# Performance work log

Measured on AMD Instinct MI355X. Metric: run time of the kernel, lower is better.

## Reference

```python
import jax, jax.numpy as jnp
import numpy as np

EPS = 1e-5
GROUPS = 16


def _deform_conv_gn(input, offset, mask, weight, bias, gamma, beta):
    # Modulated deformable conv v2 (k=3, stride=1, pad=1) + GroupNorm(16).
    B, C, H, W = input.shape
    Co = weight.shape[0]
    K = 9
    # kernel taps relative to center (pad=1 cancels the -1 origin shift)
    ky = jnp.repeat(jnp.arange(3) - 1, 3).astype(input.dtype)   # [9]
    kx = jnp.tile(jnp.arange(3) - 1, 3).astype(input.dtype)     # [9]
    off = offset.reshape(B, K, 2, H, W)                          # (dy, dx) per tap
    dy, dx = off[:, :, 0], off[:, :, 1]                          # [B,9,H,W]
    y = jnp.arange(H, dtype=input.dtype)[None, None, :, None] + ky[None, :, None, None] + dy
    x = jnp.arange(W, dtype=input.dtype)[None, None, None, :] + kx[None, :, None, None] + dx
    y0 = jnp.floor(y)
    x0 = jnp.floor(x)
    flat = input.reshape(B, C, H * W)

    def corner(yc, xc):
        # zero-padded bilinear corner gather -> [B,C,9,H,W]
        valid = ((yc >= 0) & (yc < H) & (xc >= 0) & (xc < W)).astype(input.dtype)
        yi = jnp.clip(yc, 0, H - 1).astype(jnp.int32)
        xi = jnp.clip(xc, 0, W - 1).astype(jnp.int32)
        idx = (yi * W + xi).reshape(B, -1)
        g = jax.vmap(lambda im, ix: jnp.take(im, ix, axis=1))(flat, idx)
        return g.reshape(B, C, K, H, W) * valid[:, None]

    wy1 = y - y0
    wx1 = x - x0
    wy0 = 1.0 - wy1
    wx0 = 1.0 - wx1
    val = (corner(y0, x0) * (wy0 * wx0)[:, None]
           + corner(y0, x0 + 1.0) * (wy0 * wx1)[:, None]
           + corner(y0 + 1.0, x0) * (wy1 * wx0)[:, None]
           + corner(y0 + 1.0, x0 + 1.0) * (wy1 * wx1)[:, None])
    cols = val * mask[:, None]                                   # modulation [B,C,9,H,W]
    out = jnp.einsum('bckhw,ock->bohw', cols, weight.reshape(Co, C, K))
    out = out + bias[None, :, None, None]
    # GroupNorm(16)
    g = out.reshape(B, GROUPS, Co // GROUPS, H, W)
    mu = g.mean(axis=(2, 3, 4), keepdims=True)
    var = g.var(axis=(2, 3, 4), keepdims=True)
    g = (g - mu) * jax.lax.rsqrt(var + EPS)
    return g.reshape(B, Co, H, W) * gamma[None, :, None, None] + beta[None, :, None, None]


def setup_inputs() -> dict:
    key = jax.random.key(0)
    k1, k2, k3, k4 = jax.random.split(key, 4)
    B, C, Co, H, W = 4, 256, 256, 64, 64
    return {
        'input': jax.random.normal(k1, (B, C, H, W), dtype=jnp.float32),
        'offset': jax.random.normal(k2, (B, 18, H, W), dtype=jnp.float32),
        'mask': jax.random.uniform(k3, (B, 9, H, W), dtype=jnp.float32),
        'weight': jax.random.normal(k4, (Co, C, 3, 3), dtype=jnp.float32) * 0.02,
        'bias': jnp.zeros((Co,), dtype=jnp.float32),
        'gamma': jnp.ones((Co,), dtype=jnp.float32),
        'beta': jnp.zeros((Co,), dtype=jnp.float32),
    }


def reference(input, offset, mask, weight, bias, gamma, beta):
    return _deform_conv_gn(input, offset, mask, weight, bias, gamma, beta)
```

## Files before the change

kernel.cpp:

```cpp
#include <hip/hip_runtime.h>

typedef __attribute__((ext_vector_type(8))) short short8;
typedef __attribute__((ext_vector_type(4))) float f32x4;

#define Bsz 4
#define Cin 256
#define Cout 256
#define Hh 64
#define Ww 64
#define HW 4096
#define NG 16
#define EPSV 1e-5f

#define CSTR 40
#define SPAN 12
#define ROWB 4112

#define OFF_IN   0
#define SZ_IN    (SPAN * ROWB)
#define OFF_COL  49344
#define OFF_TA   54464
#define OFF_TW   56768
#define OFF_CTL  61376
#define SMEM_BYTES 61392

static __device__ __forceinline__ unsigned f2bf(float f) {
    unsigned u = __float_as_uint(f);
    return (u + 0x7fffu + ((u >> 16) & 1u)) >> 16;
}

static __device__ __forceinline__ float2 ld8(const float* p) {
    float2 v;
    __builtin_memcpy(&v, p, 8);
    return v;
}

#define BLO(u) __uint_as_float((u) << 16)
#define BHI(u) __uint_as_float((u) & 0xffff0000u)

__launch_bounds__(512)
__global__ void prep_kernel(const float* __restrict__ in,
                            const float* __restrict__ w,
                            unsigned* __restrict__ inT,
                            ushort* __restrict__ wtb,
                            float* __restrict__ stats) {
    const int t  = threadIdx.x;
    const int bx = blockIdx.x;
    if (bx < 256) {
        const int b = bx >> 6, y = bx & 63;
        const int x = t & 63, w8 = t >> 6;
        const float* src = in + (size_t)b * 256 * HW + y * 64 + x;
        unsigned* dst = inT + ((size_t)(b * 64 + y) * 128) * 64 + x;
#pragma unroll
        for (int it = 0; it < 16; it++) {
            const int pr = w8 + it * 8;
            const float a0 = src[(size_t)(2 * pr) * HW];
            const float a1 = src[(size_t)(2 * pr + 1) * HW];
            dst[(size_t)pr * 64] = f2bf(a0) | (f2bf(a1) << 16);
        }
        return;
    }
    if (bx == 256 && t < 128) stats[t] = 0.f;
    const int i = (bx - 256) * 512 + t;
    if (i >= 72 * 256 * 32) return;
    const int cl = i & 31;
    const int o  = (i >> 5) & 255;
    const int ks = i >> 13;
    const int c  = ((ks & 7) << 5) | cl;
    const int kk = ks >> 3;
    wtb[i] = (ushort)f2bf(w[((size_t)o * Cin + c) * 9 + kk]);
}

__launch_bounds__(512, 4)
__global__ void dcn_kernel(const float* __restrict__ in,
                           const unsigned* __restrict__ inT,
                           const float* __restrict__ offs,
                           const float* __restrict__ mask,
                           const ushort* __restrict__ wtb,
                           const float* __restrict__ bias,
                           float* __restrict__ out,
                           float* __restrict__ stats) {
    extern __shared__ char smem[];
    ushort* col  = (ushort*)(smem + OFF_COL);
    int2*   s_ta = (int2*)(smem + OFF_TA);
    float4* s_tw = (float4*)(smem + OFF_TW);
    int*    s_ctl = (int*)(smem + OFF_CTL);

    const int t  = threadIdx.x;
    const int bx = blockIdx.x;
    const int q  = bx & 7, r = bx >> 3;
    const int b  = q >> 1;
    const int h  = ((q & 1) << 5) | (r >> 1);
    const int wb = (r & 1) << 5;
    const int lane = t & 63;
    const int wv   = t >> 6;
    const int quad = lane >> 4;
    const int l15  = lane & 15;
    const int px   = lane & 31;
    const int hi   = lane >> 5;
    const int proff = (2 * wv + hi) * 256;

    if (t < 2) s_ctl[t] = (t == 0) ? 64 : -1;
    __syncthreads();

    int my_min = 64, my_max = -1;
    for (int j = t; j < 288; j += 512) {
        const int k = j >> 5, p = j & 31;
        const int pp = wb + p;
        const float* ob = offs + (size_t)b * 18 * HW + h * Ww + pp;
        const float dy = ob[(2 * k) * HW];
        const float dx = ob[(2 * k + 1) * HW];
        const float m  = mask[((size_t)b * 9 + k) * HW + h * Ww + pp];
        const float y = (float)h + (float)(k / 3 - 1) + dy;
        const float x = (float)pp + (float)(k % 3 - 1) + dx;
        const float y0f = floorf(y), x0f = floorf(x);
        const float ly = y - y0f, lx = x - x0f;
        const float hy = 1.f - ly, hx = 1.f - lx;
        const int y0 = (int)y0f, x0 = (int)x0f;
        const int yc0 = min(max(y0, 0), 63);
        const int yc1 = min(max(y0 + 1, 0), 63);
        const int xb  = min(max(x0, 0), 62);
        float ax = 0.f, ay = 0.f;
        if (x0 == xb) {
            ax = hx;
            ay = lx;
        } else if (x0 < xb) {
            ax = (x0 + 1 == 0) ? lx : 0.f;
        } else {
            ay = (x0 == 63) ? hx : 0.f;
        }
        const float w0 = (y0 >= 0 && y0 < 64) ? m * hy : 0.f;
        const float w1 = (y0 + 1 >= 0 && y0 + 1 < 64) ? m * ly : 0.f;
        s_ta[j] = make_int2(yc0 * ROWB + xb * 4, yc1 * ROWB + xb * 4);
        s_tw[j] = make_float4(w0 * ax, w0 * ay, w1 * ax, w1 * ay);
        my_min = min(my_min, yc0);
        my_max = max(my_max, yc1);
    }
#pragma unroll
    for (int off = 32; off; off >>= 1) {
        my_min = min(my_min, __shfl_xor(my_min, off));
        my_max = max(my_max, __shfl_xor(my_max, off));
    }
    if (lane == 0) {
        atomicMin(&s_ctl[0], my_min);
        atomicMax(&s_ctl[1], my_max);
    }
    __syncthreads();

    const int ymin = s_ctl[0];
    const bool use_lds = (s_ctl[1] - ymin + 1) <= SPAN;
    const int ybase = ymin * ROWB;

    f32x4 acc[2][2];
#pragma unroll
    for (int i = 0; i < 2; i++)
#pragma unroll
        for (int nt = 0; nt < 2; nt++) acc[i][nt] = (f32x4){0.f, 0.f, 0.f, 0.f};

    const float* inb = in + (size_t)b * Cin * HW;

#define STAGE(cc)                                                              \
    {                                                                          \
        _Pragma("unroll")                                                      \
        for (int i = 0; i < 6; i++) {                                          \
            const int g = wv * 6 + i;                                          \
            const int rr = g >> 2, seg = g & 3;                                \
            const int row = min(ymin + rr, 63);                                \
            const unsigned* src = inT +                                        \
                ((size_t)(b * 64 + row) * 128 + (cc) * 16) * 64 +              \
                seg * 256 + lane * 4;                                          \
            __builtin_amdgcn_global_load_lds(                                  \
                (const __attribute__((address_space(1))) void*)src,            \
                (__attribute__((address_space(3))) void*)(smem + OFF_IN +      \
                    rr * ROWB + seg * 1024),                                   \
                16, 0, 0);                                                     \
        }                                                                      \
    }

#define GATHER_L(kk, pk)                                                   \
    {                                                                      \
        const int2  ad = s_ta[(kk) * 32 + px];                             \
        const float4 tw = s_tw[(kk) * 32 + px];                            \
        const char* bp = smem + OFF_IN + proff - ybase;                    \
        const float2 f0 = ld8((const float*)(bp + ad.x));                  \
        const float2 f1 = ld8((const float*)(bp + ad.y));                  \
        const unsigned u00 = __float_as_uint(f0.x);                        \
        const unsigned u01 = __float_as_uint(f0.y);                        \
        const unsigned u10 = __float_as_uint(f1.x);                        \
        const unsigned u11 = __float_as_uint(f1.y);                        \
        const float v0 = tw.x * BLO(u00) + tw.y * BLO(u01) +               \
                         tw.z * BLO(u10) + tw.w * BLO(u11);                \
        const float v1 = tw.x * BHI(u00) + tw.y * BHI(u01) +               \
                         tw.z * BHI(u10) + tw.w * BHI(u11);                \
        pk = f2bf(v0) | (f2bf(v1) << 16);                                  \
    }

#define GATHER_G(cc, kk, pk)                                               \
    {                                                                      \
        const int2  ad = s_ta[(kk) * 32 + px];                             \
        const float4 tw = s_tw[(kk) * 32 + px];                            \
        const int y0r = ad.x / ROWB, x0r = (ad.x - y0r * ROWB) >> 2;       \
        const int y1r = ad.y / ROWB, x1r = (ad.y - y1r * ROWB) >> 2;       \
        const int adx = y0r * 64 + x0r, ady = y1r * 64 + x1r;              \
        const float* cb = inb + (size_t)((cc) * 32 + wv * 4 + hi * 2) * HW;\
        float vv[2];                                                       \
        _Pragma("unroll")                                                  \
        for (int j = 0; j < 2; j++) {                                      \
            const float* pl = cb + j * HW;                                 \
            const float2 g0 = ld8(pl + adx);                               \
            const float2 g1 = ld8(pl + ady);                               \
            vv[j] = tw.x * g0.x + tw.y * g0.y + tw.z * g1.x + tw.w * g1.y; \
        }                                                                  \
        pk = f2bf(vv[0]) | (f2bf(vv[1]) << 16);                           \
    }

#define FRAGS_MFMA(ks, p)                                                      \
    {                                                                          \
        const ushort* wp =                                                     \
            wtb + ((size_t)((ks) * 256 + wv * 32 + l15)) * 32 + quad * 8;      \
        const short8 a0 = *(const short8*)wp;                                  \
        const short8 a1 = *(const short8*)(wp + 16 * 32);                      \
        short8 bfr[2];                                                         \
        _Pragma("unroll")                                                      \
        for (int nt = 0; nt < 2; nt++)                                         \
            bfr[nt] = *(const short8*)&col[(p) * (32 * CSTR) +                 \
                                           (nt * 16 + l15) * CSTR + quad * 8]; \
        _Pragma("unroll")                                                      \
        for (int nt = 0; nt < 2; nt++) {                                       \
            acc[0][nt] = __builtin_amdgcn_mfma_f32_16x16x32_bf16(              \
                a0, bfr[nt], acc[0][nt], 0, 0, 0);                             \
            acc[1][nt] = __builtin_amdgcn_mfma_f32_16x16x32_bf16(              \
                a1, bfr[nt], acc[1][nt], 0, 0, 0);                             \
        }                                                                      \
    }

    unsigned pk;
    int p = 0;

    if (use_lds) {
        STAGE(0);
        __syncthreads();
        GATHER_L(0, pk);
#pragma unroll 1
        for (int s = 0; s < 72; s++) {
            const int cc = s / 9;
            const int kk = s - cc * 9;
            const int ks = kk * 8 + cc;
            *(unsigned*)&col[p * (32 * CSTR) + px * CSTR + (wv << 2) + (hi << 1)] = pk;
            __syncthreads();
            const bool bound = (kk == 8) && (s != 71);
            if (bound) {
                STAGE(cc + 1);
            } else if (s != 71) {
                GATHER_L(kk + 1, pk);
            }
            FRAGS_MFMA(ks, p);
            if (bound) {
                __syncthreads();
                GATHER_L(0, pk);
            }
            p ^= 1;
        }
    } else {
        GATHER_G(0, 0, pk);
#pragma unroll 1
        for (int s = 0; s < 72; s++) {
            const int cc = s / 9;
            const int kk = s - cc * 9;
            const int ks = kk * 8 + cc;
            *(unsigned*)&col[p * (32 * CSTR) + px * CSTR + (wv << 2) + (hi << 1)] = pk;
            __syncthreads();
            if (s < 71) {
                const int s1 = s + 1;
                const int cc1 = s1 / 9;
                GATHER_G(cc1, s1 - cc1 * 9, pk);
            }
            FRAGS_MFMA(ks, p);
            p ^= 1;
        }
    }
#undef STAGE
#undef GATHER_L
#undef GATHER_G
#undef FRAGS_MFMA

    float gs[2], gq[2];
#pragma unroll
    for (int i = 0; i < 2; i++) {
        float s = 0.f, qq = 0.f;
        const int ob = wv * 32 + i * 16 + quad * 4;
#pragma unroll
        for (int reg = 0; reg < 4; reg++) {
            const int o = ob + reg;
            const float bv = bias[o];
            float* op = out + ((size_t)(b * 256 + o)) * HW + h * Ww + wb + l15;
#pragma unroll
            for (int nt = 0; nt < 2; nt++) {
                const float v = acc[i][nt][reg] + bv;
                op[nt * 16] = v;
                s += v;
                qq += v * v;
            }
        }
        gs[i] = s; gq[i] = qq;
    }
#pragma unroll
    for (int off = 32; off; off >>= 1) {
        gs[0] += __shfl_xor(gs[0], off);
        gq[0] += __shfl_xor(gq[0], off);
        gs[1] += __shfl_xor(gs[1], off);
        gq[1] += __shfl_xor(gq[1], off);
    }
    if (lane == 0) {
#pragma unroll
        for (int i = 0; i < 2; i++) {
            const int g = wv * 2 + i;
            atomicAdd(&stats[((size_t)b * NG + g) * 2],     gs[i]);
            atomicAdd(&stats[((size_t)b * NG + g) * 2 + 1], gq[i]);
        }
    }
}

__global__ void gn_apply_kernel(float* __restrict__ x, const float* __restrict__ stats,
                                const float* __restrict__ gamma,
                                const float* __restrict__ beta) {
    const int i = blockIdx.x * 256 + threadIdx.x;
    const int plane = i >> 10;
    const int o = plane & 255;
    const int bg = plane >> 4;
    const float s = stats[bg * 2], q = stats[bg * 2 + 1];
    const float inv_n = 1.f / 65536.f;
    const float mu = s * inv_n;
    const float var = q * inv_n - mu * mu;
    const float rs = rsqrtf(var + EPSV);
    const float ga = gamma[o] * rs;
    const float be = beta[o] - mu * ga;
    float4 v = ((float4*)x)[i];
    v.x = v.x * ga + be;
    v.y = v.y * ga + be;
    v.z = v.z * ga + be;
    v.w = v.w * ga + be;
    ((float4*)x)[i] = v;
}

extern "C" void kernel_launch(void* const* d_in, const int* in_sizes, int n_in,
                              void* d_out, int out_size, void* d_ws, size_t ws_size,
                              hipStream_t stream) {
    const float* input  = (const float*)d_in[0];
    const float* offset = (const float*)d_in[1];
    const float* maskp  = (const float*)d_in[2];
    const float* weight = (const float*)d_in[3];
    const float* bias   = (const float*)d_in[4];
    const float* gamma  = (const float*)d_in[5];
    const float* beta   = (const float*)d_in[6];
    float* out = (float*)d_out;

    ushort* wtb  = (ushort*)d_ws;
    float* stats = (float*)((char*)d_ws + (size_t)Cout * Cin * 9 * sizeof(ushort));
    unsigned* inT = (unsigned*)((char*)d_ws + 1180160);

    static int attr_done = 0;
    if (!attr_done) {
        hipFuncSetAttribute((const void*)dcn_kernel,
                            hipFuncAttributeMaxDynamicSharedMemorySize, SMEM_BYTES);
        attr_done = 1;
    }

    hipLaunchKernelGGL(prep_kernel, dim3(256 + 1152), dim3(512), 0, stream,
                       input, weight, inT, wtb, stats);
    hipLaunchKernelGGL(dcn_kernel, dim3(Bsz * Hh * 2), dim3(512), SMEM_BYTES, stream,
                       input, inT, offset, maskp, wtb, bias, out, stats);
    hipLaunchKernelGGL(gn_apply_kernel, dim3((Bsz * Cout * HW / 4) / 256), dim3(256), 0,
                       stream, out, stats, gamma, beta);
}
```

Baseline: 206.2 us.

## Gather all nine taps per channel chunk before MFMA to cut barriers

Replaces the per-tap double-buffered col pipeline (one barrier per tap, 72 steps) with a per-channel-chunk schedule. All nine taps are gathered into a 9-slot col buffer, then the nine MFMA steps run, giving two barriers per chunk instead of nine-plus. The next chunk's input staging is issued during the MFMA phase. This enlarges LDS usage from about 61KB to 79KB, which may reduce occupancy, and it gives up the gather/MFMA interleaving within a chunk.

```diff
diff --git a/kernel.cpp b/kernel.cpp
--- a/kernel.cpp
+++ b/kernel.cpp
@@ -19,10 +19,10 @@
 #define OFF_IN   0
 #define SZ_IN    (SPAN * ROWB)
 #define OFF_COL  49344
-#define OFF_TA   54464
-#define OFF_TW   56768
-#define OFF_CTL  61376
-#define SMEM_BYTES 61392
+#define OFF_TA   72384
+#define OFF_TW   74688
+#define OFF_CTL  79296
+#define SMEM_BYTES 79312
 
 static __device__ __forceinline__ unsigned f2bf(float f) {
     unsigned u = __float_as_uint(f);
@@ -177,7 +177,7 @@
         }                                                                      \
     }
 
-#define GATHER_L(kk, pk)                                                   \
+#define GATHER_PUB_L(kk)                                                   \
     {                                                                      \
         const int2  ad = s_ta[(kk) * 32 + px];                             \
         const float4 tw = s_tw[(kk) * 32 + px];                            \
@@ -192,10 +192,11 @@
                          tw.z * BLO(u10) + tw.w * BLO(u11);                \
         const float v1 = tw.x * BHI(u00) + tw.y * BHI(u01) +               \
                          tw.z * BHI(u10) + tw.w * BHI(u11);                \
-        pk = f2bf(v0) | (f2bf(v1) << 16);                                  \
-    }
-
-#define GATHER_G(cc, kk, pk)                                               \
+        *(unsigned*)&col[(kk) * (32 * CSTR) + px * CSTR + (wv << 2) +      \
+                         (hi << 1)] = f2bf(v0) | (f2bf(v1) << 16);         \
+    }
+
+#define GATHER_PUB_G(cc, kk)                                               \
     {                                                                      \
         const int2  ad = s_ta[(kk) * 32 + px];                             \
         const float4 tw = s_tw[(kk) * 32 + px];                            \
@@ -211,10 +212,11 @@
             const float2 g1 = ld8(pl + ady);                               \
             vv[j] = tw.x * g0.x + tw.y * g0.y + tw.z * g1.x + tw.w * g1.y; \
         }                                                                  \
-        pk = f2bf(vv[0]) | (f2bf(vv[1]) << 16);                           \
-    }
-
-#define FRAGS_MFMA(ks, p)                                                      \
+        *(unsigned*)&col[(kk) * (32 * CSTR) + px * CSTR + (wv << 2) +      \
+                         (hi << 1)] = f2bf(vv[0]) | (f2bf(vv[1]) << 16);   \
+    }
+
+#define FRAGS_MFMA(ks, kk)                                                     \
     {                                                                          \
         const ushort* wp =                                                     \
             wtb + ((size_t)((ks) * 256 + wv * 32 + l15)) * 32 + quad * 8;      \
@@ -223,7 +225,7 @@
         short8 bfr[2];                                                         \
         _Pragma("unroll")                                                      \
         for (int nt = 0; nt < 2; nt++)                                         \
-            bfr[nt] = *(const short8*)&col[(p) * (32 * CSTR) +                 \
+            bfr[nt] = *(const short8*)&col[(kk) * (32 * CSTR) +                \
                                            (nt * 16 + l15) * CSTR + quad * 8]; \
         _Pragma("unroll")                                                      \
         for (int nt = 0; nt < 2; nt++) {                                       \
@@ -234,54 +236,33 @@
         }                                                                      \
     }
 
-    unsigned pk;
-    int p = 0;
-
     if (use_lds) {
         STAGE(0);
         __syncthreads();
-        GATHER_L(0, pk);
 #pragma unroll 1
-        for (int s = 0; s < 72; s++) {
-            const int cc = s / 9;
-            const int kk = s - cc * 9;
-            const int ks = kk * 8 + cc;
-            *(unsigned*)&col[p * (32 * CSTR) + px * CSTR + (wv << 2) + (hi << 1)] = pk;
+        for (int cc = 0; cc < 8; cc++) {
+#pragma unroll 3
+            for (int kk = 0; kk < 9; kk++) GATHER_PUB_L(kk);
             __syncthreads();
-            const bool bound = (kk == 8) && (s != 71);
-            if (bound) {
-                STAGE(cc + 1);
-            } else if (s != 71) {
-                GATHER_L(kk + 1, pk);
-            }
-            FRAGS_MFMA(ks, p);
-            if (bound) {
-                __syncthreads();
-                GATHER_L(0, pk);
-            }
-            p ^= 1;
+            if (cc < 7) STAGE(cc + 1);
+#pragma unroll 3
+            for (int kk = 0; kk < 9; kk++) FRAGS_MFMA(kk * 8 + cc, kk);
+            __syncthreads();
         }
     } else {
-        GATHER_G(0, 0, pk);
 #pragma unroll 1
-        for (int s = 0; s < 72; s++) {
-            const int cc = s / 9;
-            const int kk = s - cc * 9;
-            const int ks = kk * 8 + cc;
-            *(unsigned*)&col[p * (32 * CSTR) + px * CSTR + (wv << 2) + (hi << 1)] = pk;
+        for (int cc = 0; cc < 8; cc++) {
+#pragma unroll 1
+            for (int kk = 0; kk < 9; kk++) GATHER_PUB_G(cc, kk);
             __syncthreads();
-            if (s < 71) {
-                const int s1 = s + 1;
-                const int cc1 = s1 / 9;
-                GATHER_G(cc1, s1 - cc1 * 9, pk);
-            }
-            FRAGS_MFMA(ks, p);
-            p ^= 1;
+#pragma unroll 3
+            for (int kk = 0; kk < 9; kk++) FRAGS_MFMA(kk * 8 + cc, kk);
+            __syncthreads();
         }
     }
 #undef STAGE
-#undef GATHER_L
-#undef GATHER_G
+#undef GATHER_PUB_L
+#undef GATHER_PUB_G
 #undef FRAGS_MFMA
 
     float gs[2], gq[2];
```

After: 194.4 us. -5.8%, faster.
